# Kernel optimization log

Measured on AMD Instinct MI355X. Metric: run time of the kernel, lower is better.

## Reference

```python
import jax, jax.numpy as jnp
import numpy as np
import math

B, V, D = 16, 4096, 512
K, H = 64, 8
DK = D // H
DE = 16
DFF = 4 * D
EPS_MASK = 1e-6
EPS_DEN = 1e-8


def setup_inputs() -> dict:
    key = jax.random.key(0)
    ks = jax.random.split(key, 16)
    s = 0.02
    return {
        "x": jax.random.normal(ks[0], (B, V, D), jnp.float32),
        "assign": jax.random.uniform(ks[1], (B, V, K), jnp.float32),
        "E": jax.random.normal(ks[2], (K, DE), jnp.float32),
        "cls0": jax.random.normal(ks[3], (1, K, D), jnp.float32) * s,
        "E2D_w": jax.random.normal(ks[4], (DE, D), jnp.float32) * s,
        "E2D_b": jnp.zeros((D,), jnp.float32),
        "Wq_w": jax.random.normal(ks[5], (D, D), jnp.float32) * s,
        "Wq_b": jnp.zeros((D,), jnp.float32),
        "Wk_w": jax.random.normal(ks[6], (D, D), jnp.float32) * s,
        "Wk_b": jnp.zeros((D,), jnp.float32),
        "Wv_w": jax.random.normal(ks[7], (D, D), jnp.float32) * s,
        "Wv_b": jnp.zeros((D,), jnp.float32),
        "ln_g": jnp.ones((D,), jnp.float32),
        "ln_b": jnp.zeros((D,), jnp.float32),
        "fc1_w": jax.random.normal(ks[8], (D, DFF), jnp.float32) * s,
        "fc1_b": jnp.zeros((DFF,), jnp.float32),
        "fc2_w": jax.random.normal(ks[9], (DFF, D), jnp.float32) * s,
        "fc2_b": jnp.zeros((D,), jnp.float32),
    }


def _layernorm(x, g, b):
    mu = x.mean(-1, keepdims=True)
    var = ((x - mu) ** 2).mean(-1, keepdims=True)
    return (x - mu) / jnp.sqrt(var + 1e-5) * g + b


def reference(x, assign, E, cls0, E2D_w, E2D_b, Wq_w, Wq_b, Wk_w, Wk_b, Wv_w, Wv_b,
              ln_g, ln_b, fc1_w, fc1_b, fc2_w, fc2_b):
    # CLS tokens modulated by module embeddings: [B,K,D]
    cls = jnp.broadcast_to(cls0, (B, K, D)) + (E @ E2D_w + E2D_b)[None]

    # detached mask (transpose of assign): [B,K,V]
    mask_kv = jax.lax.stop_gradient(jnp.swapaxes(assign, 1, 2))
    count_per_k = mask_kv.sum(-1)                 # [B,K]
    empty_mask = count_per_k <= 1e-6              # [B,K]

    # projections -> heads
    q = (_layernorm(cls, ln_g, ln_b) @ Wq_w + Wq_b).reshape(B, K, H, DK)
    k = (x @ Wk_w + Wk_b).reshape(B, V, H, DK)
    v = (x @ Wv_w + Wv_b).reshape(B, V, H, DK)

    # logits [B,H,K,V]
    logits = jnp.einsum("bkhd,bvhd->bhkv", q, k) / math.sqrt(DK)
    log_mask = jnp.log(jnp.clip(mask_kv, 0.0, 1.0) + EPS_MASK)[:, None]  # [B,1,K,V]
    scores = logits + log_mask
    scores = scores - scores.max(-1, keepdims=True)
    attn = jnp.exp(scores)
    attn = attn / (attn.sum(-1, keepdims=True) + EPS_DEN)

    # weighted values, merge heads -> [B,K,D]
    m = jnp.einsum("bhkv,bvhd->bkhd", attn, v).reshape(B, K, D)

    # empty-slot fallback
    m = jnp.where(empty_mask[..., None], cls, m)

    # FFN residual (LayerNorm shared with q path); eval mode: dropout off
    h = _layernorm(m, ln_g, ln_b)
    h = jax.nn.gelu(h @ fc1_w + fc1_b, approximate=False) @ fc2_w + fc2_b
    m = m + h
    return m, count_per_k, empty_mask
```

## Files before the change

kernel.cpp:

```cpp
#include <hip/hip_runtime.h>
#include <hip/hip_bf16.h>
#include <cstdint>
#include <cmath>

#define DEV static __device__ __forceinline__

typedef __attribute__((ext_vector_type(8))) short bf16x8;
typedef __attribute__((ext_vector_type(4))) float f32x4;

DEV ushort f2bf(float f) {
    union { float f; uint32_t u; } v; v.f = f;
    uint32_t r = v.u + 0x7FFFu + ((v.u >> 16) & 1u);
    return (ushort)(r >> 16);
}
DEV uint32_t pack2bf(float lo, float hi) {
    return (uint32_t)f2bf(lo) | ((uint32_t)f2bf(hi) << 16);
}
DEV float bf2f(ushort h) {
    union { uint32_t u; float f; } v; v.u = ((uint32_t)h) << 16;
    return v.f;
}
DEV void gld16(const ushort* g, ushort* l) {
    __builtin_amdgcn_global_load_lds(
        (const __attribute__((address_space(1))) unsigned int*)g,
        (__attribute__((address_space(3))) unsigned int*)l, 16, 0, 0);
}

DEV float2 block_reduce2(float a, float b, float2* red, int tid) {
    red[tid] = make_float2(a, b);
    __syncthreads();
    for (int s2 = 128; s2 > 0; s2 >>= 1) {
        if (tid < s2) {
            float2 o = red[tid + s2];
            float2 m = red[tid];
            red[tid] = make_float2(m.x + o.x, m.y + o.y);
        }
        __syncthreads();
    }
    float2 r = red[0];
    __syncthreads();
    return r;
}

__global__ __launch_bounds__(256)
void xcast_k(const float* __restrict__ x, ushort* __restrict__ xb)
{
    const size_t i = (size_t)blockIdx.x * 256 + threadIdx.x;
    const float4* s = (const float4*)(x + i * 8);
    float4 a = s[0], b = s[1];
    uint4 o;
    o.x = pack2bf(a.x, a.y); o.y = pack2bf(a.z, a.w);
    o.z = pack2bf(b.x, b.y); o.w = pack2bf(b.z, b.w);
    *(uint4*)(xb + i * 8) = o;
}

__global__ __launch_bounds__(256)
void prep_cls_k(const float* __restrict__ E, const float* __restrict__ cls0,
                const float* __restrict__ w, const float* __restrict__ bb,
                const float* __restrict__ g, const float* __restrict__ be,
                float* __restrict__ cls, ushort* __restrict__ clsln)
{
    const int k = blockIdx.x, tid = threadIdx.x;
    __shared__ float Ek[16];
    if (tid < 16) Ek[tid] = E[k * 16 + tid];
    __syncthreads();
    float vals[2];
#pragma unroll
    for (int j = 0; j < 2; j++) {
        int d = tid + j * 256;
        float a = cls0[k * 512 + d] + bb[d];
#pragma unroll
        for (int e = 0; e < 16; e++) a += Ek[e] * w[e * 512 + d];
        vals[j] = a;
        cls[k * 512 + d] = a;
    }
    __shared__ float2 red[256];
    float2 sr = block_reduce2(vals[0] + vals[1], vals[0] * vals[0] + vals[1] * vals[1], red, tid);
    float mu = sr.x * (1.f / 512.f);
    float var = sr.y * (1.f / 512.f) - mu * mu;
    float inv = rsqrtf(var + 1e-5f);
#pragma unroll
    for (int j = 0; j < 2; j++) {
        int d = tid + j * 256;
        clsln[k * 512 + d] = f2bf((vals[j] - mu) * inv * g[d] + be[d]);
    }
}

__global__ __launch_bounds__(512)
void prep_q_k(const ushort* __restrict__ clsln, const float* __restrict__ wq,
              const float* __restrict__ wqb, ushort* __restrict__ qbf)
{
    const int kb = blockIdx.x * 4;
    const int n = threadIdx.x;
    __shared__ float Ar[4][512];
#pragma unroll
    for (int j = 0; j < 4; j++) Ar[j][n] = bf2f(clsln[(kb + j) * 512 + n]);
    __syncthreads();
    float acc[4] = {0.f, 0.f, 0.f, 0.f};
    for (int d = 0; d < 512; ++d) {
        float wv = wq[d * 512 + n];
#pragma unroll
        for (int j = 0; j < 4; j++) acc[j] += Ar[j][d] * wv;
    }
#pragma unroll
    for (int j = 0; j < 4; j++) qbf[(kb + j) * 512 + n] = f2bf(acc[j] + wqb[n]);
}

__global__ __launch_bounds__(256)
void wprep_k(const float* __restrict__ wk, const float* __restrict__ wv,
             const float* __restrict__ fc1w, const float* __restrict__ fc2w,
             const float* __restrict__ kb, const float* __restrict__ vb,
             ushort* __restrict__ wkvt, ushort* __restrict__ fc1t,
             ushort* __restrict__ fc2t, float* __restrict__ biaskv)
{
    const int id = blockIdx.x;
    if (id >= 2560) {
        int i = (id - 2560) * 256 + threadIdx.x;
        biaskv[i] = (i < 512) ? kb[i] : vb[i - 512];
        return;
    }
    const float* in; ushort* out; int R, C, bx, by;
    if (id < 256)        { in = wk;   out = wkvt;                  R = 512;  C = 512;  int t = id;        bx = t & 15; by = t >> 4; }
    else if (id < 512)   { in = wv;   out = wkvt + 512 * 512;      R = 512;  C = 512;  int t = id - 256;  bx = t & 15; by = t >> 4; }
    else if (id < 1536)  { in = fc1w; out = fc1t;                  R = 512;  C = 2048; int t = id - 512;  bx = t & 63; by = t >> 6; }
    else                 { in = fc2w; out = fc2t;                  R = 2048; C = 512;  int t = id - 1536; bx = t & 15; by = t >> 4; }
    __shared__ float T[32][33];
    const int c0 = bx * 32, r0 = by * 32;
    const int tx = threadIdx.x & 31, ty = threadIdx.x >> 5;
#pragma unroll
    for (int i = 0; i < 32; i += 8)
        T[ty + i][tx] = in[(size_t)(r0 + ty + i) * C + c0 + tx];
    __syncthreads();
#pragma unroll
    for (int i = 0; i < 32; i += 8)
        out[(size_t)(c0 + ty + i) * R + r0 + tx] = f2bf(T[tx][ty + i]);
}

__global__ __launch_bounds__(256)
void count2_k(const float* __restrict__ assign, float* __restrict__ partial)
{
    const int vt = blockIdx.x, b = blockIdx.y;
    __shared__ float T[64][65];
    const int rr = threadIdx.x >> 2, sg = threadIdx.x & 3;
    const float4* src = (const float4*)(assign + ((size_t)b * 4096 + vt * 64 + rr) * 64 + sg * 16);
    float4 a0 = src[0], a1 = src[1], a2 = src[2], a3 = src[3];
    float* tr = &T[rr][sg * 16];
    tr[0] = a0.x; tr[1] = a0.y; tr[2] = a0.z; tr[3] = a0.w;
    tr[4] = a1.x; tr[5] = a1.y; tr[6] = a1.z; tr[7] = a1.w;
    tr[8] = a2.x; tr[9] = a2.y; tr[10] = a2.z; tr[11] = a2.w;
    tr[12] = a3.x; tr[13] = a3.y; tr[14] = a3.z; tr[15] = a3.w;
    __syncthreads();
    const int k = rr;
    float ssum = 0.f;
#pragma unroll
    for (int j = 0; j < 4; j++)
#pragma unroll
        for (int t2 = 0; t2 < 4; t2++) ssum += T[sg * 16 + j * 4 + t2][k];
    ssum += __shfl_xor(ssum, 1, 64);
    ssum += __shfl_xor(ssum, 2, 64);
    if (sg == 0) partial[((size_t)b * 64 + k) * 64 + vt] = ssum;
}

__global__ __launch_bounds__(256)
void count_fin_k(const float* __restrict__ partial, float* __restrict__ cnt,
                 float* __restrict__ emp)
{
    const int i = blockIdx.x * 256 + threadIdx.x;
    const float4* p = (const float4*)(partial + (size_t)i * 64);
    float s = 0.f;
#pragma unroll
    for (int t = 0; t < 16; t++) {
        float4 f = p[t];
        s += f.x + f.y + f.z + f.w;
    }
    cnt[i] = s;
    emp[i] = (s <= 1e-6f) ? 1.f : 0.f;
}

template<int AMODE, int EPI, int SWZ, int ND, int KD, int LDK>
__global__ __launch_bounds__(512)
void gemm_k(const void* __restrict__ Ap, const ushort* __restrict__ Bt,
            const float* __restrict__ bias,
            ushort* __restrict__ o_bf, const float* __restrict__ res,
            float* __restrict__ o_f)
{
    __shared__ ushort smem[16384];
    ushort* As = smem;
    ushort* Bs = smem + 8192;
    int m0, n0;
    if (SWZ) {
        int L = blockIdx.x;
        int c = L & 7, j = L >> 3;
        m0 = (c * 64 + (j >> 3)) * 128;
        n0 = (j & 7) * 128;
    } else {
        m0 = blockIdx.x * 128;
        n0 = blockIdx.y * 128;
    }
    const int tid = threadIdx.x;
    const int w = tid >> 6, l = tid & 63;
    const int wr = w >> 2, wc = w & 3;
    const int lg = l >> 4, lr = l & 15;

    const f32x4 fzero = {0.f, 0.f, 0.f, 0.f};
    f32x4 acc[4][2];
#pragma unroll
    for (int i = 0; i < 4; i++)
#pragma unroll
        for (int j = 0; j < 2; j++) acc[i][j] = fzero;

    const int lrow8 = l >> 3;
    const int colswz = ((l & 7) ^ lrow8) * 8;
    const ushort* gB  = Bt + (size_t)(n0 + w * 16 + lrow8) * LDK + colswz;
    const ushort* gA0 = (const ushort*)Ap + (size_t)(m0 + w * 16 + lrow8) * LDK + colswz;
    const float*  gA1 = (const float*)Ap + (size_t)(m0 + w * 16 + (l >> 2)) * LDK + (l & 3) * 16;

    const int kbase = blockIdx.z * KD;
    constexpr int NT = KD / 64;
#pragma unroll
    for (int t = 0; t < NT; ++t) {
        const int kt = kbase + t * 64;
        __syncthreads();
        if (AMODE == 0) {
#pragma unroll
            for (int i = 0; i < 2; i++) {
                gld16(gA0 + (size_t)i * 8 * LDK + kt, As + (w * 16 + i * 8) * 64);
                gld16(gB + (size_t)i * 8 * LDK + kt, Bs + (w * 16 + i * 8) * 64);
            }
        } else {
            float4 av[4];
#pragma unroll
            for (int i = 0; i < 4; i++)
                av[i] = *(const float4*)(gA1 + kt + i * 4);
#pragma unroll
            for (int i = 0; i < 2; i++)
                gld16(gB + (size_t)i * 8 * LDK + kt, Bs + (w * 16 + i * 8) * 64);
            {
                int r = w * 16 + (l >> 2);
                uint2 p0, p1;
                p0.x = pack2bf(av[0].x, av[0].y); p0.y = pack2bf(av[0].z, av[0].w);
                uint2 q0; q0.x = pack2bf(av[1].x, av[1].y); q0.y = pack2bf(av[1].z, av[1].w);
                p1.x = pack2bf(av[2].x, av[2].y); p1.y = pack2bf(av[2].z, av[2].w);
                uint2 q1; q1.x = pack2bf(av[3].x, av[3].y); q1.y = pack2bf(av[3].z, av[3].w);
                int cb = (l & 3) * 32;
                *(uint2*)((char*)As + r * 128 + ((cb     ) ^ ((r & 7) << 4))) = p0;
                *(uint2*)((char*)As + r * 128 + ((cb +  8) ^ ((r & 7) << 4))) = q0;
                *(uint2*)((char*)As + r * 128 + ((cb + 16) ^ ((r & 7) << 4))) = p1;
                *(uint2*)((char*)As + r * 128 + ((cb + 24) ^ ((r & 7) << 4))) = q1;
            }
        }
        asm volatile("s_waitcnt vmcnt(0)" ::: "memory");
        __syncthreads();
#pragma unroll
        for (int kk = 0; kk < 2; kk++) {
            int kb = (kk * 32 + lg * 8) * 2;
            bf16x8 af[4], bfv[2];
#pragma unroll
            for (int mi = 0; mi < 4; mi++) {
                int row = wr * 64 + mi * 16 + lr;
                af[mi] = *(bf16x8*)((char*)As + row * 128 + (kb ^ ((row & 7) << 4)));
            }
#pragma unroll
            for (int ni = 0; ni < 2; ni++) {
                int row = wc * 32 + ni * 16 + lr;
                bfv[ni] = *(bf16x8*)((char*)Bs + row * 128 + (kb ^ ((row & 7) << 4)));
            }
#pragma unroll
            for (int mi = 0; mi < 4; mi++)
#pragma unroll
                for (int ni = 0; ni < 2; ni++)
                    acc[mi][ni] = __builtin_amdgcn_mfma_f32_16x16x32_bf16(af[mi], bfv[ni], acc[mi][ni], 0, 0, 0);
        }
    }

    if (EPI == 0) {
        __syncthreads();
#pragma unroll
        for (int mi = 0; mi < 4; mi++)
#pragma unroll
            for (int ni = 0; ni < 2; ni++)
#pragma unroll
                for (int r = 0; r < 4; r++) {
                    int rl = wr * 64 + mi * 16 + lg * 4 + r;
                    int cl = wc * 32 + ni * 16 + lr;
                    int byteoff = rl * 256 + ((cl * 2) ^ ((rl & 7) << 4));
                    *(ushort*)((char*)smem + byteoff) = f2bf(acc[mi][ni][r] + bias[n0 + cl]);
                }
        __syncthreads();
        const int row = tid >> 2, sg2 = tid & 3;
        uint4* dq = (uint4*)(o_bf + (size_t)(m0 + row) * ND + n0 + sg2 * 32);
#pragma unroll
        for (int q2 = 0; q2 < 4; q2++) {
            int byteoff = row * 256 + ((sg2 * 64 + q2 * 16) ^ ((row & 7) << 4));
            dq[q2] = *(const uint4*)((char*)smem + byteoff);
        }
    } else {
        float* ofz = o_f;
        if (EPI == 3)
            ofz = o_f + (size_t)blockIdx.z * (size_t)gridDim.x * 128 * ND;
#pragma unroll
        for (int mi = 0; mi < 4; mi++) {
#pragma unroll
            for (int ni = 0; ni < 2; ni++) {
#pragma unroll
                for (int r = 0; r < 4; r++) {
                    int row = m0 + wr * 64 + mi * 16 + lg * 4 + r;
                    int col = n0 + wc * 32 + ni * 16 + lr;
                    if (EPI == 1) {
                        float c = acc[mi][ni][r] + bias[col];
                        float gg = 0.5f * c * (1.f + erff(c * 0.70710678f));
                        o_bf[(size_t)row * ND + col] = f2bf(gg);
                    } else if (EPI == 2) {
                        float c = acc[mi][ni][r] + bias[col];
                        o_f[(size_t)row * ND + col] = c + res[(size_t)row * ND + col];
                    } else {
                        ofz[(size_t)row * ND + col] = acc[mi][ni][r];
                    }
                }
            }
        }
    }
}

__global__ __launch_bounds__(256)
void combine2_k(const float* __restrict__ fcp, const float* __restrict__ fc2b,
                float* __restrict__ mout)
{
    const int i = blockIdx.x * 256 + threadIdx.x;
    const int col = i & 511;
    float s = fc2b[col] + fcp[i] + fcp[i + 524288] + fcp[i + 2 * 524288] + fcp[i + 3 * 524288];
    mout[i] += s;
}

__global__ __launch_bounds__(256)
void attn_k(const ushort* __restrict__ qbf, const ushort* __restrict__ kv,
            const float* __restrict__ assign,
            float* __restrict__ partO, float* __restrict__ partML)
{
    const int s = blockIdx.x, h = blockIdx.y, b = blockIdx.z;
    __shared__ ushort Qs[64 * 64];
    __shared__ ushort Ks[64 * 64];
    __shared__ ushort Vt[64 * 64];
    __shared__ ushort Ps[64 * 64];
    __shared__ float  Lm[64 * 64];
    const int tid = threadIdx.x;
    const int w = tid >> 6, l = tid & 63, lg = l >> 4, lr = l & 15;
    const int rr = tid >> 2, qt = tid & 3;

    {
        const uint4* src = (const uint4*)(qbf + rr * 512 + h * 64 + qt * 16);
        uint4 t0 = src[0], t1 = src[1];
        int kb = qt * 32;
        *(uint4*)((char*)Qs + rr * 128 + ( kb       ^ ((rr & 7) << 4))) = t0;
        *(uint4*)((char*)Qs + rr * 128 + ((kb + 16) ^ ((rr & 7) << 4))) = t1;
    }

    const f32x4 fzero = {0.f, 0.f, 0.f, 0.f};
    f32x4 oacc[4];
#pragma unroll
    for (int ni = 0; ni < 4; ni++) oacc[ni] = fzero;
    float m_run[4], l_run[4];
#pragma unroll
    for (int r = 0; r < 4; r++) { m_run[r] = -3e38f; l_run[r] = 0.f; }

    const int v00 = s * 512;

    for (int c = 0; c < 8; ++c) {
        const int vb = v00 + c * 64;
        __syncthreads();
        {
            const size_t rowb = ((size_t)b * 4096 + vb + rr) * 1024 + h * 64;
            const uint4* srck = (const uint4*)(kv + rowb + qt * 16);
            uint4 k0 = srck[0], k1 = srck[1];
            int kb = qt * 32;
            *(uint4*)((char*)Ks + rr * 128 + ( kb       ^ ((rr & 7) << 4))) = k0;
            *(uint4*)((char*)Ks + rr * 128 + ((kb + 16) ^ ((rr & 7) << 4))) = k1;
            const ushort* srcv = kv + rowb + 512 + qt * 16;
            ushort vvv[16];
            *(uint4*)&vvv[0] = ((const uint4*)srcv)[0];
            *(uint4*)&vvv[8] = ((const uint4*)srcv)[1];
#pragma unroll
            for (int i = 0; i < 16; i++) {
                int dk = qt * 16 + i;
                *(ushort*)((char*)Vt + dk * 128 + ((rr * 2) ^ ((dk & 7) << 4))) = vvv[i];
            }
            const float4* srca = (const float4*)(assign + ((size_t)b * 4096 + vb + rr) * 64 + qt * 16);
            float4 A0 = srca[0], A1 = srca[1], A2 = srca[2], A3 = srca[3];
            float av[16] = {A0.x, A0.y, A0.z, A0.w, A1.x, A1.y, A1.z, A1.w,
                            A2.x, A2.y, A2.z, A2.w, A3.x, A3.y, A3.z, A3.w};
#pragma unroll
            for (int i = 0; i < 16; i++)
                Lm[(qt * 16 + i) * 64 + rr] = __logf(fminf(fmaxf(av[i], 0.f), 1.f) + 1e-6f);
        }
        __syncthreads();

        f32x4 sacc[4];
#pragma unroll
        for (int ni = 0; ni < 4; ni++) sacc[ni] = fzero;
#pragma unroll
        for (int kk = 0; kk < 2; kk++) {
            int kb = (kk * 32 + lg * 8) * 2;
            int qrow = w * 16 + lr;
            bf16x8 aq = *(bf16x8*)((char*)Qs + qrow * 128 + (kb ^ ((qrow & 7) << 4)));
#pragma unroll
            for (int ni = 0; ni < 4; ni++) {
                int kr = ni * 16 + lr;
                bf16x8 bk = *(bf16x8*)((char*)Ks + kr * 128 + (kb ^ ((kr & 7) << 4)));
                sacc[ni] = __builtin_amdgcn_mfma_f32_16x16x32_bf16(aq, bk, sacc[ni], 0, 0, 0);
            }
        }
        float sv[4][4], mx[4];
#pragma unroll
        for (int r = 0; r < 4; r++) {
            int q = w * 16 + lg * 4 + r;
            float m_ = -3e38f;
#pragma unroll
            for (int ni = 0; ni < 4; ni++) {
                float xx = sacc[ni][r] * 0.125f + Lm[q * 64 + ni * 16 + lr];
                sv[ni][r] = xx;
                m_ = fmaxf(m_, xx);
            }
            mx[r] = m_;
        }
#pragma unroll
        for (int off = 1; off < 16; off <<= 1)
#pragma unroll
            for (int r = 0; r < 4; r++) mx[r] = fmaxf(mx[r], __shfl_xor(mx[r], off, 64));
        float scale[4], lad[4];
#pragma unroll
        for (int r = 0; r < 4; r++) {
            float mn = fmaxf(m_run[r], mx[r]);
            scale[r] = __expf(m_run[r] - mn);
            m_run[r] = mn;
            float ls = 0.f;
#pragma unroll
            for (int ni = 0; ni < 4; ni++) {
                float p = __expf(sv[ni][r] - mn);
                sv[ni][r] = p;
                ls += p;
            }
            lad[r] = ls;
        }
#pragma unroll
        for (int off = 1; off < 16; off <<= 1)
#pragma unroll
            for (int r = 0; r < 4; r++) lad[r] += __shfl_xor(lad[r], off, 64);
#pragma unroll
        for (int r = 0; r < 4; r++) l_run[r] = l_run[r] * scale[r] + lad[r];
#pragma unroll
        for (int ni = 0; ni < 4; ni++) {
            f32x4 o = oacc[ni];
            o[0] *= scale[0]; o[1] *= scale[1]; o[2] *= scale[2]; o[3] *= scale[3];
            oacc[ni] = o;
        }
#pragma unroll
        for (int ni = 0; ni < 4; ni++)
#pragma unroll
            for (int r = 0; r < 4; r++) {
                int q = w * 16 + lg * 4 + r;
                int key = ni * 16 + lr;
                *(ushort*)((char*)Ps + q * 128 + ((key * 2) ^ ((q & 7) << 4))) = f2bf(sv[ni][r]);
            }
#pragma unroll
        for (int kk = 0; kk < 2; kk++) {
            int kb = (kk * 32 + lg * 8) * 2;
            int prow = w * 16 + lr;
            bf16x8 ap = *(bf16x8*)((char*)Ps + prow * 128 + (kb ^ ((prow & 7) << 4)));
#pragma unroll
            for (int ni = 0; ni < 4; ni++) {
                int dk = ni * 16 + lr;
                bf16x8 bv = *(bf16x8*)((char*)Vt + dk * 128 + (kb ^ ((dk & 7) << 4)));
                oacc[ni] = __builtin_amdgcn_mfma_f32_16x16x32_bf16(ap, bv, oacc[ni], 0, 0, 0);
            }
        }
    }
    const size_t ob = ((size_t)((b * 8 + h) * 8 + s)) * 4096;
#pragma unroll
    for (int ni = 0; ni < 4; ni++)
#pragma unroll
        for (int r = 0; r < 4; r++) {
            int q = w * 16 + lg * 4 + r;
            int dk = ni * 16 + lr;
            partO[ob + q * 64 + dk] = oacc[ni][r];
        }
    if (lr == 0) {
#pragma unroll
        for (int r = 0; r < 4; r++) {
            int q = w * 16 + lg * 4 + r;
            partML[((b * 8 + h) * 8 + s) * 128 + q * 2 + 0] = m_run[r];
            partML[((b * 8 + h) * 8 + s) * 128 + q * 2 + 1] = l_run[r];
        }
    }
}

__global__ __launch_bounds__(256)
void combine_k(const float* __restrict__ partO, const float* __restrict__ partML,
               const float* __restrict__ cls, const float* __restrict__ cnt,
               float* __restrict__ mout)
{
    const int bh = blockIdx.x, b = bh >> 3, h = bh & 7;
    __shared__ float Ms[64], Ls[64];
    const int tid = threadIdx.x;
    if (tid < 64) {
        float M = -3e38f;
#pragma unroll
        for (int s2 = 0; s2 < 8; s2++) M = fmaxf(M, partML[(bh * 8 + s2) * 128 + tid * 2]);
        float L = 0.f;
#pragma unroll
        for (int s2 = 0; s2 < 8; s2++) {
            float m_ = partML[(bh * 8 + s2) * 128 + tid * 2];
            float l_ = partML[(bh * 8 + s2) * 128 + tid * 2 + 1];
            L += l_ * __expf(m_ - M);
        }
        Ms[tid] = M; Ls[tid] = L;
    }
    __syncthreads();
#pragma unroll
    for (int i = 0; i < 16; i++) {
        int e = i * 256 + tid;
        int q = e >> 6, dk = e & 63;
        float o = 0.f;
#pragma unroll
        for (int s2 = 0; s2 < 8; s2++) {
            float m_ = partML[(bh * 8 + s2) * 128 + q * 2];
            o += partO[(size_t)(bh * 8 + s2) * 4096 + e] * __expf(m_ - Ms[q]);
        }
        float val = o / (Ls[q] + 1e-8f);
        if (cnt[b * 64 + q] <= 1e-6f) val = cls[q * 512 + h * 64 + dk];
        mout[((size_t)b * 64 + q) * 512 + h * 64 + dk] = val;
    }
}

__global__ __launch_bounds__(256)
void ln_rows_k(const float* __restrict__ m, const float* __restrict__ g,
               const float* __restrict__ be, ushort* __restrict__ out)
{
    const int r = blockIdx.x, tid = threadIdx.x;
    float v0 = m[(size_t)r * 512 + tid];
    float v1 = m[(size_t)r * 512 + tid + 256];
    __shared__ float2 red[256];
    float2 sr = block_reduce2(v0 + v1, v0 * v0 + v1 * v1, red, tid);
    float mu = sr.x * (1.f / 512.f);
    float var = sr.y * (1.f / 512.f) - mu * mu;
    float inv = rsqrtf(var + 1e-5f);
    out[(size_t)r * 512 + tid]       = f2bf((v0 - mu) * inv * g[tid] + be[tid]);
    out[(size_t)r * 512 + tid + 256] = f2bf((v1 - mu) * inv * g[tid + 256] + be[tid + 256]);
}

extern "C" void kernel_launch(void* const* d_in, const int* in_sizes, int n_in,
                              void* d_out, int out_size, void* d_ws, size_t ws_size,
                              hipStream_t stream)
{
    const float* x      = (const float*)d_in[0];
    const float* assign = (const float*)d_in[1];
    const float* E      = (const float*)d_in[2];
    const float* cls0   = (const float*)d_in[3];
    const float* e2dw   = (const float*)d_in[4];
    const float* e2db   = (const float*)d_in[5];
    const float* wq     = (const float*)d_in[6];
    const float* wqb    = (const float*)d_in[7];
    const float* wk     = (const float*)d_in[8];
    const float* wkb    = (const float*)d_in[9];
    const float* wv     = (const float*)d_in[10];
    const float* wvb    = (const float*)d_in[11];
    const float* lng    = (const float*)d_in[12];
    const float* lnbv   = (const float*)d_in[13];
    const float* fc1w   = (const float*)d_in[14];
    const float* fc1b   = (const float*)d_in[15];
    const float* fc2w   = (const float*)d_in[16];
    const float* fc2b   = (const float*)d_in[17];

    float* mout = (float*)d_out;
    float* cnt  = mout + (size_t)16 * 64 * 512;
    float* emp  = cnt + 16 * 64;

    char* ws = (char*)d_ws;
    size_t off = 0;
    auto alloc = [&](size_t bytes) -> char* {
        char* p = ws + off;
        off = (off + bytes + 255) & ~(size_t)255;
        return p;
    };
    float*  cls    = (float*) alloc((size_t)64 * 512 * 4);
    ushort* clsln  = (ushort*)alloc((size_t)64 * 512 * 2);
    ushort* qbf    = (ushort*)alloc((size_t)64 * 512 * 2);
    ushort* wkvt   = (ushort*)alloc((size_t)1024 * 512 * 2);
    float*  biaskv = (float*) alloc((size_t)1024 * 4);
    ushort* fc1t   = (ushort*)alloc((size_t)2048 * 512 * 2);
    ushort* fc2t   = (ushort*)alloc((size_t)512 * 2048 * 2);
    ushort* kvb    = (ushort*)alloc((size_t)16 * 4096 * 1024 * 2);
    float*  partO  = (float*) alloc((size_t)16 * 8 * 8 * 64 * 64 * 4);
    float*  partML = (float*) alloc((size_t)16 * 8 * 8 * 64 * 2 * 4);
    float*  cpart  = (float*) alloc((size_t)16 * 64 * 64 * 4);
    ushort* lnbf   = (ushort*)alloc((size_t)1024 * 512 * 2);
    ushort* hhb    = (ushort*)alloc((size_t)1024 * 2048 * 2);
    float*  fcp    = (float*) alloc((size_t)4 * 1024 * 512 * 4);
    ushort* xb     = (ushort*)alloc((size_t)16 * 4096 * 512 * 2);
    const bool use_xb = (off <= ws_size);

    prep_cls_k<<<64, 256, 0, stream>>>(E, cls0, e2dw, e2db, lng, lnbv, cls, clsln);
    prep_q_k<<<16, 512, 0, stream>>>(clsln, wq, wqb, qbf);
    wprep_k<<<2564, 256, 0, stream>>>(wk, wv, fc1w, fc2w, wkb, wvb,
                                      wkvt, fc1t, fc2t, biaskv);
    count2_k<<<dim3(64, 16), 256, 0, stream>>>(assign, cpart);
    count_fin_k<<<4, 256, 0, stream>>>(cpart, cnt, emp);

    if (use_xb) {
        xcast_k<<<16384, 256, 0, stream>>>(x, xb);
        gemm_k<0, 0, 1, 1024, 512, 512><<<4096, 512, 0, stream>>>(xb, wkvt, biaskv,
                                                                  kvb, nullptr, nullptr);
    } else {
        gemm_k<1, 0, 1, 1024, 512, 512><<<4096, 512, 0, stream>>>(x, wkvt, biaskv,
                                                                  kvb, nullptr, nullptr);
    }
    attn_k<<<dim3(8, 8, 16), 256, 0, stream>>>(qbf, kvb, assign, partO, partML);
    combine_k<<<128, 256, 0, stream>>>(partO, partML, cls, cnt, mout);
    ln_rows_k<<<1024, 256, 0, stream>>>(mout, lng, lnbv, lnbf);
    gemm_k<0, 1, 0, 2048, 512, 512><<<dim3(8, 16), 512, 0, stream>>>(lnbf, fc1t, fc1b,
                                                                     hhb, nullptr, nullptr);
    gemm_k<0, 3, 0, 512, 512, 2048><<<dim3(8, 4, 4), 512, 0, stream>>>(hhb, fc2t, fc2b,
                                                                       nullptr, nullptr, fcp);
    combine2_k<<<2048, 256, 0, stream>>>(fcp, fc2b, mout);
}
```

Before: 299.8 us.

## Use 256x128 tile GEMM for K/V projection to increase operand reuse

Adds a dedicated bf16 GEMM kernel for the K/V projection with 256-row by 128-column block tiles, where each of 8 waves computes a 64x64 sub-tile with 16 accumulators. The grid is halved. Each loaded B tile is reused across twice as many rows, which cuts global/L2 traffic for the weight operand. The trade-off is more LDS per block, more accumulator registers, lower occupancy, and fewer blocks to cover the GPU. The epilogue is staged through swizzled LDS in two halves.

```diff
diff --git a/kernel.cpp b/kernel.cpp
--- a/kernel.cpp
+++ b/kernel.cpp
@@ -175,6 +175,93 @@
     }
     cnt[i] = s;
     emp[i] = (s <= 1e-6f) ? 1.f : 0.f;
+}
+
+__global__ __launch_bounds__(512)
+void gemm256_k(const ushort* __restrict__ Ap, const ushort* __restrict__ Bt,
+               const float* __restrict__ bias, ushort* __restrict__ o_bf)
+{
+    __shared__ ushort smem[24576];
+    ushort* As = smem;
+    ushort* Bs = smem + 16384;
+    const int L = blockIdx.x;
+    const int c = L & 7, j = L >> 3;
+    const int m0 = (c * 32 + (j >> 3)) * 256;
+    const int n0 = (j & 7) * 128;
+    const int tid = threadIdx.x;
+    const int w = tid >> 6, l = tid & 63;
+    const int wr = w >> 1, wc = w & 1;
+    const int lg = l >> 4, lr = l & 15;
+
+    const f32x4 fzero = {0.f, 0.f, 0.f, 0.f};
+    f32x4 acc[4][4];
+#pragma unroll
+    for (int i = 0; i < 4; i++)
+#pragma unroll
+        for (int jj = 0; jj < 4; jj++) acc[i][jj] = fzero;
+
+    const int lrow8 = l >> 3;
+    const int colswz = ((l & 7) ^ lrow8) * 8;
+    const ushort* gA = Ap + (size_t)(m0 + w * 32 + lrow8) * 512 + colswz;
+    const ushort* gB = Bt + (size_t)(n0 + w * 16 + lrow8) * 512 + colswz;
+
+    for (int t = 0; t < 8; ++t) {
+        const int kt = t * 64;
+        __syncthreads();
+#pragma unroll
+        for (int i = 0; i < 4; i++)
+            gld16(gA + (size_t)i * 8 * 512 + kt, As + (w * 32 + i * 8) * 64);
+#pragma unroll
+        for (int i = 0; i < 2; i++)
+            gld16(gB + (size_t)i * 8 * 512 + kt, Bs + (w * 16 + i * 8) * 64);
+        asm volatile("s_waitcnt vmcnt(0)" ::: "memory");
+        __syncthreads();
+#pragma unroll
+        for (int kk = 0; kk < 2; kk++) {
+            int kb = (kk * 32 + lg * 8) * 2;
+            bf16x8 af[4], bfv[4];
+#pragma unroll
+            for (int mi = 0; mi < 4; mi++) {
+                int row = wr * 64 + mi * 16 + lr;
+                af[mi] = *(bf16x8*)((char*)As + row * 128 + (kb ^ ((row & 7) << 4)));
+            }
+#pragma unroll
+            for (int ni = 0; ni < 4; ni++) {
+                int row = wc * 64 + ni * 16 + lr;
+                bfv[ni] = *(bf16x8*)((char*)Bs + row * 128 + (kb ^ ((row & 7) << 4)));
+            }
+#pragma unroll
+            for (int mi = 0; mi < 4; mi++)
+#pragma unroll
+                for (int ni = 0; ni < 4; ni++)
+                    acc[mi][ni] = __builtin_amdgcn_mfma_f32_16x16x32_bf16(af[mi], bfv[ni], acc[mi][ni], 0, 0, 0);
+        }
+    }
+#pragma unroll
+    for (int h2 = 0; h2 < 2; ++h2) {
+        __syncthreads();
+        if ((wr >> 1) == h2) {
+#pragma unroll
+            for (int mi = 0; mi < 4; mi++)
+#pragma unroll
+                for (int ni = 0; ni < 4; ni++)
+#pragma unroll
+                    for (int r = 0; r < 4; r++) {
+                        int rl = (wr & 1) * 64 + mi * 16 + lg * 4 + r;
+                        int cl = wc * 64 + ni * 16 + lr;
+                        int byteoff = rl * 256 + ((cl * 2) ^ ((rl & 7) << 4));
+                        *(ushort*)((char*)smem + byteoff) = f2bf(acc[mi][ni][r] + bias[n0 + cl]);
+                    }
+        }
+        __syncthreads();
+        const int row = tid >> 2, sg2 = tid & 3;
+        uint4* dq = (uint4*)(o_bf + (size_t)(m0 + h2 * 128 + row) * 1024 + n0 + sg2 * 32);
+#pragma unroll
+        for (int q2 = 0; q2 < 4; q2++) {
+            int byteoff = row * 256 + ((sg2 * 64 + q2 * 16) ^ ((row & 7) << 4));
+            dq[q2] = *(const uint4*)((char*)smem + byteoff);
+        }
+    }
 }
 
 template<int AMODE, int EPI, int SWZ, int ND, int KD, int LDK>
@@ -607,8 +694,7 @@
 
     if (use_xb) {
         xcast_k<<<16384, 256, 0, stream>>>(x, xb);
-        gemm_k<0, 0, 1, 1024, 512, 512><<<4096, 512, 0, stream>>>(xb, wkvt, biaskv,
-                                                                  kvb, nullptr, nullptr);
+        gemm256_k<<<2048, 512, 0, stream>>>(xb, wkvt, biaskv, kvb);
     } else {
         gemm_k<1, 0, 1, 1024, 512, 512><<<4096, 512, 0, stream>>>(x, wkvt, biaskv,
                                                                   kvb, nullptr, nullptr);
```

New measurement: 308.5 us. 1.03x slower.
